# Kernel optimization log

Hardware: AMD Instinct MI355X
Metric: run time of the kernel (lower is better)

The kernel has to match this reference:

```python
import jax, jax.numpy as jnp
import numpy as np

EPS_NORM = 1e-12
EPS_ABS = 1e-12


def _stack3(x):
    # x: [B, T, C] -> [B, T, 3, C] with left-shift, identity, right-shift taps
    prev = jnp.pad(x[:, :-1, :], ((0, 0), (1, 0), (0, 0)))
    nxt = jnp.pad(x[:, 1:, :], ((0, 0), (0, 1), (0, 0)))
    return jnp.stack([prev, x, nxt], axis=2)


def _l2_norm(x, axis):
    # matches layer's l2_normal: sqrt(max(sum(x^2), eps)), keepdims
    sq = jnp.sum(jnp.square(x), axis=axis, keepdims=True)
    return jnp.sqrt(jnp.maximum(sq, EPS_NORM))


def setup_inputs() -> dict:
    key = jax.random.key(0)
    k1, k2 = jax.random.split(key)
    B, T, C, K, U = 32, 4096, 128, 3, 256
    inputs = jax.random.normal(k1, (B, T, C), dtype=jnp.float32)
    # glorot uniform for w: limit = sqrt(6/(fan_in+fan_out)) with fan_in=C*K, fan_out=U
    limit = np.sqrt(6.0 / (C * K + U)).astype(np.float32)
    w = jax.random.uniform(k2, (1, C * K, U), dtype=jnp.float32, minval=-limit, maxval=limit)
    b = jnp.zeros((U,), dtype=jnp.float32)
    p = jnp.ones((U,), dtype=jnp.float32)
    q = jnp.zeros((1,), dtype=jnp.float32)
    return {"inputs": inputs, "w": w, "b": b, "p": p, "q": q}


def reference(inputs, w, b, p, q):
    B, T, C = inputs.shape
    U = w.shape[-1]
    x = _stack3(inputs).reshape(B, T, 3 * C)          # [B, T, 3C] (tap-major, matches tf stack+reshape)
    q2 = jnp.square(q)                                 # [1]
    x_norm = _l2_norm(x, axis=2) + q2                  # [B, T, 1]
    w_norm = _l2_norm(w, axis=1) + q2                  # [1, 1, U]
    w2 = w[0]                                          # [3C, U]
    sign = jnp.sign(jnp.einsum('btk,ku->btu', x, w2))  # sign of raw matmul
    y = jnp.einsum('btk,ku->btu', x / x_norm, w2 / w_norm[0])
    y = jnp.abs(y) + EPS_ABS
    y = jnp.power(y, jnp.square(p))                    # broadcast over units
    y = sign * y + b
    return y
```

## Files before the change

### kernel.cpp

```cpp
#include <hip/hip_runtime.h>

typedef __attribute__((ext_vector_type(8))) short short8;
typedef __attribute__((ext_vector_type(4))) float f32x4;

#define T_DIM 4096
#define C_DIM 128
#define U_DIM 256
#define BM 64
#define NROWS 66
#define LDK 136
#define NT 8

__device__ __forceinline__ unsigned short f2bf(float f) {
    unsigned int u = __float_as_uint(f);
    u += 0x7FFFu + ((u >> 16) & 1u);
    return (unsigned short)(u >> 16);
}

__global__ void prep_kernel(const float* __restrict__ w,
                            const float* __restrict__ b,
                            const float* __restrict__ p,
                            const float* __restrict__ q,
                            unsigned short* __restrict__ wfrag,
                            float* __restrict__ winv,
                            float* __restrict__ p2,
                            float* __restrict__ bc) {
    if (blockIdx.x < 48) {
        int idx = blockIdx.x * 256 + threadIdx.x;
        int l  = idx & 63;
        int nt = (idx >> 6) & 15;
        int ks = idx >> 10;
        int n  = nt * 16 + (l & 15);
        int k0 = ks * 32 + ((l >> 4) << 3);
        #pragma unroll
        for (int j = 0; j < 8; ++j) {
            wfrag[(size_t)idx * 8 + j] = f2bf(w[(k0 + j) * U_DIM + n]);
        }
    } else {
        int u = threadIdx.x;
        float ss = 0.f;
        for (int k = 0; k < 3 * C_DIM; ++k) {
            float v = w[k * U_DIM + u];
            ss += v * v;
        }
        float q2 = q[0] * q[0];
        winv[u] = 1.0f / (sqrtf(fmaxf(ss, 1e-12f)) + q2);
        float pv = p[u];
        p2[u] = pv * pv;
        bc[u] = b[u];
    }
}

#define STAGE_LOAD(t0v, vv)                                                    \
    do {                                                                       \
        _Pragma("unroll")                                                      \
        for (int i_ = 0; i_ < 9; ++i_) {                                       \
            int r_ = r0 + i_ * 8;                                              \
            int t_ = (t0v) + r_ - 1;                                           \
            float4 val_ = make_float4(0.f, 0.f, 0.f, 0.f);                     \
            if (r_ < NROWS && (unsigned)t_ < T_DIM)                            \
                val_ = *(const float4*)(inp + ((size_t)bb * T_DIM + t_) * C_DIM + lc); \
            vv[i_] = val_;                                                     \
        }                                                                      \
    } while (0)

#define STAGE_WRITE(vv, buf)                                                   \
    do {                                                                       \
        _Pragma("unroll")                                                      \
        for (int i_ = 0; i_ < 9; ++i_) {                                       \
            int r_ = r0 + i_ * 8;                                              \
            if (r_ < NROWS) {                                                  \
                float4 val_ = vv[i_];                                          \
                float part_ = val_.x * val_.x + val_.y * val_.y                \
                            + val_.z * val_.z + val_.w * val_.w;               \
                _Pragma("unroll")                                              \
                for (int o_ = 16; o_ > 0; o_ >>= 1)                            \
                    part_ += __shfl_xor(part_, o_, 32);                        \
                if ((tid & 31) == 0) ss_s[buf][r_] = part_;                    \
                ushort4 sv_;                                                   \
                sv_.x = f2bf(val_.x); sv_.y = f2bf(val_.y);                    \
                sv_.z = f2bf(val_.z); sv_.w = f2bf(val_.w);                    \
                *(ushort4*)(&inp_s[buf][r_][lc]) = sv_;                        \
            }                                                                  \
        }                                                                      \
    } while (0)

__global__ __launch_bounds__(256, 2) void cossim_main(
        const float* __restrict__ inp,
        const unsigned short* __restrict__ wfrag,
        const float* __restrict__ winv,
        const float* __restrict__ p2g,
        const float* __restrict__ bg,
        const float* __restrict__ qg,
        float* __restrict__ out) {
    __shared__ unsigned short inp_s[2][NROWS][LDK];
    __shared__ float ss_s[2][NROWS];

    const int tid = threadIdx.x;
    int bid = blockIdx.x;
    bid = (bid & 7) * 64 + (bid >> 3);
    const int bb = bid >> 4;
    const int tg = (bid >> 1) & 7;
    const int uh = bid & 1;

    const int wid = tid >> 6;
    const int l   = tid & 63;
    const int l15 = l & 15;
    const int lg  = l >> 4;
    const int r0  = tid >> 5;
    const int lc  = (tid & 31) * 4;

    const float q2 = qg[0] * qg[0];
    const short8* wf = (const short8*)wfrag;

    short8 wr[12][2];
    #pragma unroll
    for (int ks = 0; ks < 12; ++ks)
        #pragma unroll
        for (int uf = 0; uf < 2; ++uf)
            wr[ks][uf] = wf[(size_t)(ks * 16 + uh * 8 + wid * 2 + uf) * 64 + l];

    const int ucb = uh * 128 + wid * 32;
    f32x4 wiv[2], ppv[2], bbv[2];
    #pragma unroll
    for (int uf = 0; uf < 2; ++uf) {
        int uc = ucb + uf * 16 + lg * 4;
        wiv[uf] = *(const f32x4*)(winv + uc);
        ppv[uf] = *(const f32x4*)(p2g + uc);
        bbv[uf] = *(const f32x4*)(bg + uc);
    }

    const int tbase = tg * (NT * BM);
    {
        float4 v0[9];
        STAGE_LOAD(tbase, v0);
        STAGE_WRITE(v0, 0);
    }
    __syncthreads();

    int cur = 0;
    for (int it = 0; it < NT; ++it) {
        const int t0 = tbase + it * BM;

        float4 vn[9];
        if (it + 1 < NT) STAGE_LOAD(t0 + BM, vn);

        f32x4 acc[4][2];
        #pragma unroll
        for (int tf = 0; tf < 4; ++tf)
            #pragma unroll
            for (int uf = 0; uf < 2; ++uf)
                acc[tf][uf] = (f32x4){0.f, 0.f, 0.f, 0.f};

        #pragma unroll
        for (int ks = 0; ks < 12; ++ks) {
            const int tap = ks >> 2;
            const int c0  = (ks & 3) * 32 + lg * 8;
            short8 xv[4];
            #pragma unroll
            for (int tf = 0; tf < 4; ++tf)
                xv[tf] = *(const short8*)(&inp_s[cur][tf * 16 + l15 + tap][c0]);
            #pragma unroll
            for (int tf = 0; tf < 4; ++tf)
                #pragma unroll
                for (int uf = 0; uf < 2; ++uf)
                    acc[tf][uf] = __builtin_amdgcn_mfma_f32_16x16x32_bf16(
                        wr[ks][uf], xv[tf], acc[tf][uf], 0, 0, 0);
        }

        float xi[4];
        #pragma unroll
        for (int tf = 0; tf < 4; ++tf) {
            int trow = tf * 16 + l15;
            float s3 = ss_s[cur][trow] + ss_s[cur][trow + 1] + ss_s[cur][trow + 2];
            xi[tf] = 1.0f / (sqrtf(fmaxf(s3, 1e-12f)) + q2);
        }

        if (it + 1 < NT) STAGE_WRITE(vn, cur ^ 1);
        __syncthreads();

        #pragma unroll
        for (int tf = 0; tf < 4; ++tf) {
            float* orow = out + ((size_t)bb * T_DIM + t0 + tf * 16 + l15) * U_DIM;
            #pragma unroll
            for (int uf = 0; uf < 2; ++uf) {
                f32x4 r;
                #pragma unroll
                for (int j = 0; j < 4; ++j) {
                    float raw = acc[tf][uf][j];
                    float y   = raw * xi[tf] * wiv[uf][j];
                    float ay  = fabsf(y) + 1e-12f;
                    float pw  = ppv[uf][j];
                    float rr  = (pw == 1.0f) ? ay : exp2f(pw * __log2f(ay));
                    r[j] = __builtin_copysignf(rr, raw) + bbv[uf][j];
                }
                *(f32x4*)(orow + ucb + uf * 16 + lg * 4) = r;
            }
        }

        cur ^= 1;
    }
}

extern "C" void kernel_launch(void* const* d_in, const int* in_sizes, int n_in,
                              void* d_out, int out_size, void* d_ws, size_t ws_size,
                              hipStream_t stream) {
    const float* inp = (const float*)d_in[0];
    const float* w   = (const float*)d_in[1];
    const float* b   = (const float*)d_in[2];
    const float* p   = (const float*)d_in[3];
    const float* q   = (const float*)d_in[4];
    float* out = (float*)d_out;

    unsigned short* wfrag = (unsigned short*)d_ws;
    float* winv = (float*)((char*)d_ws + 196608);
    float* p2   = winv + 256;
    float* bc   = p2 + 256;

    prep_kernel<<<49, 256, 0, stream>>>(w, b, p, q, wfrag, winv, p2, bc);
    cossim_main<<<512, 256, 0, stream>>>(inp, wfrag, winv, p2, bc, q, out);
}
```

Measured before the change: 63.55 us.

## Use 1024-thread blocks covering all 256 units to share input tiles

Each block now spans all 256 output units with 16 waves of 16 units each, instead of two blocks each handling half of the units. Each staged input tile is therefore loaded and converted once rather than twice, which halves global input traffic and the per-row norm work. The grid drops to 256 blocks and the per-thread loads to 3 rows. In exchange, 256 blocks may underfill the 256 CUs, and the larger blocks synchronise more threads at each barrier. Each wave also issues half as many MFMAs per LDS fragment read, so reuse of fragments held in registers drops.

```diff
diff --git a/kernel.cpp b/kernel.cpp
--- a/kernel.cpp
+++ b/kernel.cpp
@@ -54,8 +54,8 @@
 #define STAGE_LOAD(t0v, vv)                                                    \
     do {                                                                       \
         _Pragma("unroll")                                                      \
-        for (int i_ = 0; i_ < 9; ++i_) {                                       \
-            int r_ = r0 + i_ * 8;                                              \
+        for (int i_ = 0; i_ < 3; ++i_) {                                       \
+            int r_ = r0 + i_ * 32;                                             \
             int t_ = (t0v) + r_ - 1;                                           \
             float4 val_ = make_float4(0.f, 0.f, 0.f, 0.f);                     \
             if (r_ < NROWS && (unsigned)t_ < T_DIM)                            \
@@ -67,8 +67,8 @@
 #define STAGE_WRITE(vv, buf)                                                   \
     do {                                                                       \
         _Pragma("unroll")                                                      \
-        for (int i_ = 0; i_ < 9; ++i_) {                                       \
-            int r_ = r0 + i_ * 8;                                              \
+        for (int i_ = 0; i_ < 3; ++i_) {                                       \
+            int r_ = r0 + i_ * 32;                                             \
             if (r_ < NROWS) {                                                  \
                 float4 val_ = vv[i_];                                          \
                 float part_ = val_.x * val_.x + val_.y * val_.y                \
@@ -85,7 +85,7 @@
         }                                                                      \
     } while (0)
 
-__global__ __launch_bounds__(256, 2) void cossim_main(
+__global__ __launch_bounds__(1024, 4) void cossim_main(
         const float* __restrict__ inp,
         const unsigned short* __restrict__ wfrag,
         const float* __restrict__ winv,
@@ -97,11 +97,9 @@
     __shared__ float ss_s[2][NROWS];
 
     const int tid = threadIdx.x;
-    int bid = blockIdx.x;
-    bid = (bid & 7) * 64 + (bid >> 3);
-    const int bb = bid >> 4;
-    const int tg = (bid >> 1) & 7;
-    const int uh = bid & 1;
+    const int bid = blockIdx.x;
+    const int bb  = bid >> 3;
+    const int tg  = bid & 7;
 
     const int wid = tid >> 6;
     const int l   = tid & 63;
@@ -113,26 +111,23 @@
     const float q2 = qg[0] * qg[0];
     const short8* wf = (const short8*)wfrag;
 
-    short8 wr[12][2];
+    short8 wr[12];
     #pragma unroll
     for (int ks = 0; ks < 12; ++ks)
-        #pragma unroll
-        for (int uf = 0; uf < 2; ++uf)
-            wr[ks][uf] = wf[(size_t)(ks * 16 + uh * 8 + wid * 2 + uf) * 64 + l];
-
-    const int ucb = uh * 128 + wid * 32;
-    f32x4 wiv[2], ppv[2], bbv[2];
-    #pragma unroll
-    for (int uf = 0; uf < 2; ++uf) {
-        int uc = ucb + uf * 16 + lg * 4;
-        wiv[uf] = *(const f32x4*)(winv + uc);
-        ppv[uf] = *(const f32x4*)(p2g + uc);
-        bbv[uf] = *(const f32x4*)(bg + uc);
+        wr[ks] = wf[(size_t)(ks * 16 + wid) * 64 + l];
+
+    const int ucb = wid * 16;
+    f32x4 wiv, ppv, bbv;
+    {
+        int uc = ucb + lg * 4;
+        wiv = *(const f32x4*)(winv + uc);
+        ppv = *(const f32x4*)(p2g + uc);
+        bbv = *(const f32x4*)(bg + uc);
     }
 
     const int tbase = tg * (NT * BM);
     {
-        float4 v0[9];
+        float4 v0[3];
         STAGE_LOAD(tbase, v0);
         STAGE_WRITE(v0, 0);
     }
@@ -142,15 +137,13 @@
     for (int it = 0; it < NT; ++it) {
         const int t0 = tbase + it * BM;
 
-        float4 vn[9];
+        float4 vn[3];
         if (it + 1 < NT) STAGE_LOAD(t0 + BM, vn);
 
-        f32x4 acc[4][2];
+        f32x4 acc[4];
         #pragma unroll
         for (int tf = 0; tf < 4; ++tf)
-            #pragma unroll
-            for (int uf = 0; uf < 2; ++uf)
-                acc[tf][uf] = (f32x4){0.f, 0.f, 0.f, 0.f};
+            acc[tf] = (f32x4){0.f, 0.f, 0.f, 0.f};
 
         #pragma unroll
         for (int ks = 0; ks < 12; ++ks) {
@@ -162,10 +155,8 @@
                 xv[tf] = *(const short8*)(&inp_s[cur][tf * 16 + l15 + tap][c0]);
             #pragma unroll
             for (int tf = 0; tf < 4; ++tf)
-                #pragma unroll
-                for (int uf = 0; uf < 2; ++uf)
-                    acc[tf][uf] = __builtin_amdgcn_mfma_f32_16x16x32_bf16(
-                        wr[ks][uf], xv[tf], acc[tf][uf], 0, 0, 0);
+                acc[tf] = __builtin_amdgcn_mfma_f32_16x16x32_bf16(
+                    wr[ks], xv[tf], acc[tf], 0, 0, 0);
         }
 
         float xi[4];
@@ -182,20 +173,17 @@
         #pragma unroll
         for (int tf = 0; tf < 4; ++tf) {
             float* orow = out + ((size_t)bb * T_DIM + t0 + tf * 16 + l15) * U_DIM;
+            f32x4 r;
             #pragma unroll
-            for (int uf = 0; uf < 2; ++uf) {
-                f32x4 r;
-                #pragma unroll
-                for (int j = 0; j < 4; ++j) {
-                    float raw = acc[tf][uf][j];
-                    float y   = raw * xi[tf] * wiv[uf][j];
-                    float ay  = fabsf(y) + 1e-12f;
-                    float pw  = ppv[uf][j];
-                    float rr  = (pw == 1.0f) ? ay : exp2f(pw * __log2f(ay));
-                    r[j] = __builtin_copysignf(rr, raw) + bbv[uf][j];
-                }
-                *(f32x4*)(orow + ucb + uf * 16 + lg * 4) = r;
+            for (int j = 0; j < 4; ++j) {
+                float raw = acc[tf][j];
+                float y   = raw * xi[tf] * wiv[j];
+                float ay  = fabsf(y) + 1e-12f;
+                float pw  = ppv[j];
+                float rr  = (pw == 1.0f) ? ay : exp2f(pw * __log2f(ay));
+                r[j] = __builtin_copysignf(rr, raw) + bbv[j];
             }
+            *(f32x4*)(orow + ucb + lg * 4) = r;
         }
 
         cur ^= 1;
@@ -218,5 +206,5 @@
     float* bc   = p2 + 256;
 
     prep_kernel<<<49, 256, 0, stream>>>(w, b, p, q, wfrag, winv, p2, bc);
-    cossim_main<<<512, 256, 0, stream>>>(inp, wfrag, winv, p2, bc, q, out);
-}
+    cossim_main<<<256, 1024, 0, stream>>>(inp, wfrag, winv, p2, bc, q, out);
+}
```

Measured after the change: 70.11 us. 1.1x slower.
